# Kernel tuning notes

Measured on AMD Instinct MI355X. Metric: run time of the kernel, lower is better.

Reference implementation:

```python
import jax, jax.numpy as jnp
import numpy as np

C = 256
SCALE = 2
K = 3
GROUPS = 4


def _conv(x, w, b=None, groups=1, pad=0):
    y = jax.lax.conv_general_dilated(
        x, w, window_strides=(1, 1), padding=[(pad, pad), (pad, pad)],
        dimension_numbers=("NCHW", "OIHW", "NCHW"), feature_group_count=groups)
    if b is not None:
        y = y + b[None, :, None, None]
    return y


def _bn(x, g, b, m, v):
    # eval-mode BatchNorm2d, eps=1e-5
    scale = g / jnp.sqrt(v + 1e-5)
    return (x - m[None, :, None, None]) * scale[None, :, None, None] + b[None, :, None, None]


def _silu(x):
    return x * jax.nn.sigmoid(x)


def setup_inputs() -> dict:
    key = jax.random.key(0)
    ks = jax.random.split(key, 16)
    c = C
    s2k2 = SCALE ** 2 * K ** 2
    p = lambda k, shape, sc=0.05: jax.random.normal(k, shape, dtype=jnp.float32) * sc
    return {
        "x": jax.random.normal(ks[0], (8, c, 64, 64), dtype=jnp.float32),
        # kernel_compressor: 1x1, c -> c//2
        "Wkc": p(ks[1], (c // 2, c, 1, 1)), "bkc": p(ks[2], (c // 2,)),
        # kernel_predictor: 3x3 c//2 -> c//4, BN, SiLU, 1x1 -> s^2*k^2
        "Wkp1": p(ks[3], (c // 4, c // 2, 3, 3)), "bkp1": p(ks[4], (c // 4,)),
        "g1": 1.0 + p(ks[5], (c // 4,)), "be1": p(ks[6], (c // 4,)),
        "m1": p(ks[7], (c // 4,)), "v1": 1.0 + jax.random.uniform(ks[8], (c // 4,), dtype=jnp.float32),
        "Wkp2": p(ks[9], (s2k2, c // 4, 1, 1)), "bkp2": p(ks[10], (s2k2,)),
        # grouped 3x3 "deform" conv: c -> c, groups=4, no bias
        "Wdef": p(ks[11], (c, c // GROUPS, 3, 3)),
        # semantic gate
        "Wg1": p(ks[12], (c // 4, c, 1, 1)), "bg1": p(ks[13], (c // 4,)),
        "Wg2": p(ks[14], (c, c // 4, 1, 1)), "bg2": p(ks[15], (c,)),
    }


def reference(x, Wkc, bkc, Wkp1, bkp1, g1, be1, m1, v1, Wkp2, bkp2, Wdef, Wg1, bg1, Wg2, bg2):
    b, c, h, w = x.shape
    s, k = SCALE, K
    # --- dynamic reassembly kernel prediction ---
    comp = _conv(x, Wkc, bkc)                                    # (b, c/2, h, w)
    t = _silu(_bn(_conv(comp, Wkp1, bkp1, pad=1), g1, be1, m1, v1))
    kw = _conv(t, Wkp2, bkp2)                                    # (b, s^2*k^2, h, w)
    kw = kw.transpose(0, 2, 3, 1).reshape(b, h, w, s * s, k * k)
    kw = jax.nn.softmax(kw, axis=-1)
    # --- unfold (k x k patches, pad k//2), F.unfold ordering: kernel pos i*k+j ---
    xp = jnp.pad(x, ((0, 0), (0, 0), (1, 1), (1, 1)))
    patches = jnp.stack([xp[:, :, i:i + h, j:j + w]
                         for i in range(k) for j in range(k)], axis=-1)  # (b,c,h,w,k^2)
    kernel_out = jnp.einsum('bchwk,bhwsk->bhwsc', patches, kw)           # (b,h,w,s^2,c)
    kernel_out = kernel_out.transpose(0, 4, 1, 3, 2).reshape(b, c, h * s, w * s)
    # --- grouped conv branch + bilinear upsample (align_corners=False) ---
    enh = _conv(x, Wdef, None, groups=GROUPS, pad=1)
    up = jax.image.resize(enh, (b, c, h * s, w * s), method='linear')
    fused = kernel_out + up
    # --- SE-style semantic gate ---
    pooled = jnp.mean(fused, axis=(2, 3), keepdims=True)
    gate = jax.nn.sigmoid(_conv(_silu(_conv(pooled, Wg1, bg1)), Wg2, bg2))
    return fused * gate
```

## Files before the change

### kernel.cpp

```cpp
#include <hip/hip_runtime.h>
#include <hip/hip_bf16.h>

typedef __hip_bfloat16 bf16;
typedef __attribute__((ext_vector_type(8))) short short8;
typedef __attribute__((ext_vector_type(4))) float floatx4;

__device__ __forceinline__ float cvt(float v){ return v; }
__device__ __forceinline__ float cvt(bf16 v){ return __bfloat162float(v); }
__device__ __forceinline__ unsigned short f2bu(float f){
    union { float f; unsigned u; } uf; uf.f = f;
    unsigned u = uf.u;
    return (unsigned short)((u + 0x7FFFu + ((u>>16)&1u)) >> 16);
}
__device__ __forceinline__ float bu2f(unsigned short b){
    union { unsigned u; float f; } uf; uf.u = ((unsigned)b)<<16; return uf.f;
}
__device__ __forceinline__ floatx4 mfma16(short8 a, short8 b, floatx4 c){
    return __builtin_amdgcn_mfma_f32_16x16x32_bf16(a, b, c, 0, 0, 0);
}
__device__ __forceinline__ int swz8(int row, int part){
    return row*32 + ((part ^ ((row>>1)&3))<<3);
}
template<typename T>
__device__ __forceinline__ void ld4(const T* p, float& o0, float& o1, float& o2, float& o3){
    T t[4]; __builtin_memcpy(t, p, 4*sizeof(T));
    o0=cvt(t[0]); o1=cvt(t[1]); o2=cvt(t[2]); o3=cvt(t[3]);
}
__device__ __forceinline__ void ld2f(const float* p, float& o0, float& o1){
    float t[2]; __builtin_memcpy(t, p, 8);
    o0=t[0]; o1=t[1];
}

constexpr size_t O_KW    = 0;
constexpr size_t O_ENH   = O_KW    + 1179648;
constexpr size_t O_XBT   = O_ENH   + 8388608;
constexpr size_t O_COMPB = O_XBT   + 4194304;
constexpr size_t O_TB    = O_COMPB + 2097152;
constexpr size_t O_POOL  = O_TB    + 1048576;
constexpr size_t O_GATE  = O_POOL  + 2048;
constexpr size_t O_WKC   = O_GATE  + 2048;
constexpr size_t O_BKC   = O_WKC   + 32768;
constexpr size_t O_WKP1  = O_BKC   + 128;
constexpr size_t O_ALPHA = O_WKP1  + 73728;
constexpr size_t O_BETA  = O_ALPHA + 64;
constexpr size_t O_WKP2  = O_BETA  + 64;
constexpr size_t O_BKP2  = O_WKP2  + 2304;
constexpr size_t O_WDEF  = O_BKP2  + 64;
constexpr size_t O_WG1   = O_WDEF  + 147456;
constexpr size_t O_BG1   = O_WG1   + 16384;
constexpr size_t O_WG2   = O_BG1   + 64;
constexpr size_t O_BG2   = O_WG2   + 16384;
constexpr size_t O_FLAG  = O_BG2   + 256;
constexpr size_t O_WKCB  = (O_FLAG + 1 + 3) & ~(size_t)3;
constexpr size_t O_WKP1B = O_WKCB  + 16384;
constexpr size_t O_WDEFB = O_WKP1B + 36864;

__global__ __launch_bounds__(256) void kdet(const unsigned* __restrict__ w, float* flag)
{
    int hits = 0;
    for (int i = threadIdx.x; i < 16384; i += 256){
        unsigned v = w[i];
        hits += (((v >> 7) & 0xFFu) == 0xFFu) ? 1 : 0;
    }
    __shared__ int sh[256];
    sh[threadIdx.x] = hits;
    __syncthreads();
    for (int o = 128; o > 0; o >>= 1){
        if (threadIdx.x < o) sh[threadIdx.x] += sh[threadIdx.x + o];
        __syncthreads();
    }
    if (threadIdx.x == 0) flag[0] = (sh[0] > 0) ? 1.0f : 0.0f;
}

template<typename T>
__device__ __forceinline__ void k0_body(
    const T* Wkc, const T* bkc, const T* Wkp1, const T* bkp1,
    const T* g1, const T* be1, const T* m1, const T* v1,
    const T* Wkp2, const T* bkp2, const T* Wdef,
    const T* Wg1, const T* bg1, const T* Wg2, const T* bg2,
    float* ws)
{
    int i = blockIdx.x*256 + threadIdx.x;
    if (i < 32768){ ws[O_WKC+i] = cvt(Wkc[i]); return; }  i -= 32768;
    if (i < 128)  { ws[O_BKC+i] = cvt(bkc[i]); return; }  i -= 128;
    if (i < 73728){ ws[O_WKP1+i]= cvt(Wkp1[i]); return; } i -= 73728;
    if (i < 64){
        float a = cvt(g1[i]) / sqrtf(cvt(v1[i]) + 1e-5f);
        ws[O_ALPHA+i] = a;
        ws[O_BETA+i]  = (cvt(bkp1[i]) - cvt(m1[i]))*a + cvt(be1[i]);
        return;
    } i -= 64;
    if (i < 2304) { ws[O_WKP2+i] = cvt(Wkp2[i]); return; } i -= 2304;
    if (i < 36)   { ws[O_BKP2+i] = cvt(bkp2[i]); return; } i -= 36;
    if (i < 147456){ ws[O_WDEF+i]= cvt(Wdef[i]); return; } i -= 147456;
    if (i < 16384){ ws[O_WG1+i]  = cvt(Wg1[i]); return; }  i -= 16384;
    if (i < 64)   { ws[O_BG1+i]  = cvt(bg1[i]); return; }  i -= 64;
    if (i < 16384){ ws[O_WG2+i]  = cvt(Wg2[i]); return; }  i -= 16384;
    if (i < 256)  { ws[O_BG2+i]  = cvt(bg2[i]); return; }  i -= 256;
    if (i < 2048) { ws[O_POOL+i] = 0.f; return; }
}

__global__ __launch_bounds__(256) void k0_prep(
    const void* Wkc, const void* bkc, const void* Wkp1, const void* bkp1,
    const void* g1, const void* be1, const void* m1, const void* v1,
    const void* Wkp2, const void* bkp2, const void* Wdef,
    const void* Wg1, const void* bg1, const void* Wg2, const void* bg2,
    float* ws)
{
    if (ws[O_FLAG] > 0.5f)
        k0_body<float>((const float*)Wkc,(const float*)bkc,(const float*)Wkp1,(const float*)bkp1,
                       (const float*)g1,(const float*)be1,(const float*)m1,(const float*)v1,
                       (const float*)Wkp2,(const float*)bkp2,(const float*)Wdef,
                       (const float*)Wg1,(const float*)bg1,(const float*)Wg2,(const float*)bg2, ws);
    else
        k0_body<bf16>((const bf16*)Wkc,(const bf16*)bkc,(const bf16*)Wkp1,(const bf16*)bkp1,
                      (const bf16*)g1,(const bf16*)be1,(const bf16*)m1,(const bf16*)v1,
                      (const bf16*)Wkp2,(const bf16*)bkp2,(const bf16*)Wdef,
                      (const bf16*)Wg1,(const bf16*)bg1,(const bf16*)Wg2,(const bf16*)bg2, ws);
}

__global__ __launch_bounds__(256) void k0b_pack(float* ws)
{
    unsigned short* wkcb  = (unsigned short*)(ws + O_WKCB);
    unsigned short* wkp1b = (unsigned short*)(ws + O_WKP1B);
    unsigned short* wdefb = (unsigned short*)(ws + O_WDEFB);
    int i = blockIdx.x*256 + threadIdx.x;
    if (i < 32768){
        int kc = i>>12, cout = (i>>5)&127, cil = i&31;
        wkcb[i] = f2bu(ws[O_WKC + (size_t)cout*256 + kc*32 + cil]);
        return;
    } i -= 32768;
    if (i < 73728){
        int ch = i/18432, r = i - ch*18432;
        int kp = r>>11, cout = (r>>5)&63, cil = r&31;
        wkp1b[i] = f2bu(ws[O_WKP1 + ((size_t)cout*128 + ch*32 + cil)*9 + kp]);
        return;
    } i -= 73728;
    if (i < 147456){
        int g = i/36864, r1 = i - g*36864;
        int ch = r1/18432, r2 = r1 - ch*18432;
        int kp = r2>>11, cout = (r2>>5)&63, cil = r2&31;
        wdefb[i] = f2bu(ws[O_WDEF + (((size_t)(g*64+cout))*64 + ch*32 + cil)*9 + kp]);
    }
}

template<typename T>
__device__ __forceinline__ void xcvt_body(const T* __restrict__ x, unsigned short* __restrict__ xbt,
                                          float* lT)
{
    const int b = blockIdx.y;
    const int ci0 = (blockIdx.x & 3) * 64;
    const int pos0 = (blockIdx.x >> 2) * 64;
    const int lane = threadIdx.x & 63;
    const int wrow = threadIdx.x >> 6;
    for (int i = wrow; i < 64; i += 4)
        lT[i*65 + lane] = cvt(x[((size_t)(b*256 + ci0 + i))*4096 + pos0 + lane]);
    __syncthreads();
    for (int u = threadIdx.x; u < 2048; u += 256){
        const int pr = u >> 5, pc = u & 31;
        unsigned lo = f2bu(lT[(2*pc)*65 + pr]);
        unsigned hi = f2bu(lT[(2*pc+1)*65 + pr]);
        *(unsigned*)&xbt[((size_t)(b*4096) + pos0 + pr)*256 + ci0 + 2*pc] = lo | (hi<<16);
    }
}

__global__ __launch_bounds__(256) void xcvt(const void* x, unsigned short* xbt, const float* flag)
{
    __shared__ float lT[64*65];
    if (*flag > 0.5f) xcvt_body<float>((const float*)x, xbt, lT);
    else              xcvt_body<bf16>((const bf16*)x, xbt, lT);
}

__global__ __launch_bounds__(256) void k1_mfma(
    const unsigned short* __restrict__ xbt, const unsigned short* __restrict__ wb,
    const float* __restrict__ bias, unsigned short* __restrict__ compb)
{
    __shared__ __align__(16) short lA[128*32];
    __shared__ __align__(16) short lB[64*32];
    const int b = blockIdx.y, pos0 = blockIdx.x*64;
    const int tid = threadIdx.x;
    const int wave = tid>>6, lane = tid&63, q = lane>>4, r16 = lane&15;
    const int mh = (wave&1)*64, nh = (wave>>1)*32;
    floatx4 zero = {0.f,0.f,0.f,0.f};
    floatx4 acc[4][2];
    #pragma unroll
    for (int m=0;m<4;m++){ acc[m][0]=zero; acc[m][1]=zero; }

    for (int kc=0;kc<8;kc++){
        __syncthreads();
        {
            const short8* s = (const short8*)(wb + kc*4096);
            const int u0 = tid, u1 = tid + 256;
            *(short8*)&lA[swz8(u0>>2, u0&3)] = s[u0];
            *(short8*)&lA[swz8(u1>>2, u1&3)] = s[u1];
        }
        {
            const int p = tid>>2, part = tid&3;
            *(short8*)&lB[swz8(p, part)] =
                *(const short8*)(xbt + ((size_t)(b*4096)+pos0+p)*256 + kc*32 + part*8);
        }
        __syncthreads();
        short8 af[4], bfr[2];
        #pragma unroll
        for (int mt=0;mt<4;mt++) af[mt]  = *(const short8*)&lA[swz8(mh + mt*16 + r16, q)];
        #pragma unroll
        for (int nt=0;nt<2;nt++) bfr[nt] = *(const short8*)&lB[swz8(nh + nt*16 + r16, q)];
        #pragma unroll
        for (int mt=0;mt<4;mt++)
            #pragma unroll
            for (int nt=0;nt<2;nt++)
                acc[mt][nt] = mfma16(af[mt], bfr[nt], acc[mt][nt]);
    }
    #pragma unroll
    for (int mt=0;mt<4;mt++){
        const int cb = mh + mt*16 + q*4;
        const float b0=bias[cb], b1=bias[cb+1], b2=bias[cb+2], b3=bias[cb+3];
        #pragma unroll
        for (int nt=0;nt<2;nt++){
            const int pos = pos0 + nh + nt*16 + r16;
            floatx4 v = acc[mt][nt];
            uint2 pk;
            pk.x = (unsigned)f2bu(v.x+b0) | ((unsigned)f2bu(v.y+b1)<<16);
            pk.y = (unsigned)f2bu(v.z+b2) | ((unsigned)f2bu(v.w+b3)<<16);
            *(uint2*)(compb + ((size_t)(b*4096)+pos)*128 + cb) = pk;
        }
    }
}

__global__ __launch_bounds__(256) void conv3x3_all(
    const unsigned short* __restrict__ xbt, const unsigned short* __restrict__ compb,
    const unsigned short* __restrict__ wkp1b, const unsigned short* __restrict__ wdefb,
    const float* __restrict__ alpha, const float* __restrict__ beta,
    const float* __restrict__ Wkp2, const float* __restrict__ bkp2,
    float* __restrict__ kw, float* __restrict__ enh)
{
    __shared__ __align__(16) short lXT[18432];
    __shared__ float wl[2340];
    const int row0 = blockIdx.x*4, b = blockIdx.y, z = blockIdx.z;
    const bool isKP = (z == 0);
    const int g = isKP ? 0 : (z-1);
    const int CICH  = isKP ? 4 : 2;
    const int CITOT = isKP ? 128 : 256;
    const int cibase = g*64;
    const unsigned short* src  = isKP ? compb : xbt;
    const unsigned short* wsrc = isKP ? wkp1b : (wdefb + (size_t)g*36864);
    const int tid = threadIdx.x;
    const int wave = tid>>6, lane = tid&63, q = lane>>4, r16 = lane&15;
    floatx4 zero = {0.f,0.f,0.f,0.f};
    floatx4 acc[4][4];
    #pragma unroll
    for (int m=0;m<4;m++){ acc[m][0]=zero; acc[m][1]=zero; acc[m][2]=zero; acc[m][3]=zero; }

    {
        short8 zz = {0,0,0,0,0,0,0,0};
        short8* d = (short8*)lXT;
        for (int i = tid; i < 1584; i += 256) d[i] = zz;
    }
    if (isKP){
        for (int i = tid; i < 2340; i += 256)
            wl[i] = (i < 2304) ? Wkp2[i] : bkp2[i-2304];
    }

    for (int ch = 0; ch < CICH; ch++){
        __syncthreads();
        {
            const int gc = tid>>2, part = tid&3;
            #pragma unroll
            for (int r=0;r<6;r++){
                const int gr = row0 - 1 + r;
                if ((unsigned)gr < 64u){
                    const unsigned short* sp = src +
                        ((size_t)(b*4096) + gr*64 + gc)*CITOT + cibase + ch*32 + part*8;
                    *(short8*)&lXT[swz8(r*66 + 1 + gc, part)] = *(const short8*)sp;
                }
            }
        }
        __syncthreads();
        const unsigned short* wch = wsrc + ch*18432;
        #pragma unroll
        for (int kp=0; kp<9; kp++){
            const int dr = kp/3, dc = kp - dr*3;
            short8 af[4], bfr[4];
            #pragma unroll
            for (int mt=0;mt<4;mt++)
                af[mt] = *(const short8*)(wch + (kp*64 + mt*16 + r16)*32 + q*8);
            #pragma unroll
            for (int nt=0;nt<4;nt++)
                bfr[nt] = *(const short8*)&lXT[swz8((wave+dr)*66 + nt*16 + r16 + dc, q)];
            #pragma unroll
            for (int mt=0;mt<4;mt++)
                #pragma unroll
                for (int nt=0;nt<4;nt++)
                    acc[mt][nt] = mfma16(af[mt], bfr[nt], acc[mt][nt]);
        }
    }
    if (isKP){
        __syncthreads();
        #pragma unroll
        for (int mt=0;mt<4;mt++){
            const int cb = mt*16 + q*4;
            const float a0=alpha[cb],a1=alpha[cb+1],a2=alpha[cb+2],a3=alpha[cb+3];
            const float e0=beta[cb],e1=beta[cb+1],e2=beta[cb+2],e3=beta[cb+3];
            #pragma unroll
            for (int nt=0;nt<4;nt++){
                const int pl = wave*64 + nt*16 + r16;
                floatx4 v = acc[mt][nt];
                float z0=v.x*a0+e0, z1=v.y*a1+e1, z2=v.z*a2+e2, z3=v.w*a3+e3;
                z0 = z0/(1.f+expf(-z0)); z1 = z1/(1.f+expf(-z1));
                z2 = z2/(1.f+expf(-z2)); z3 = z3/(1.f+expf(-z3));
                uint2 pk;
                pk.x = (unsigned)f2bu(z0) | ((unsigned)f2bu(z1)<<16);
                pk.y = (unsigned)f2bu(z2) | ((unsigned)f2bu(z3)<<16);
                *(uint2*)&lXT[pl*72 + cb] = pk;
            }
        }
        __syncthreads();
        const unsigned short* tp = (const unsigned short*)&lXT[tid*72];
        float acc36[36];
        #pragma unroll
        for (int o=0;o<36;o++) acc36[o] = wl[2304+o];
        #pragma unroll
        for (int c8=0;c8<8;c8++){
            short8 v8 = *(const short8*)(tp + c8*8);
            float f[8];
            #pragma unroll
            for (int j=0;j<8;j++) f[j] = bu2f((unsigned short)v8[j]);
            #pragma unroll
            for (int jj=0;jj<8;jj++){
                const int ci = c8*8+jj;
                #pragma unroll
                for (int o=0;o<36;o++) acc36[o] += f[jj]*wl[o*64+ci];
            }
        }
        const int gid = b*4096 + (row0 + (tid>>6))*64 + (tid&63);
        float* op = kw + (size_t)gid*36;
        #pragma unroll
        for (int s=0;s<4;s++){
            float mx = acc36[s*9];
            #pragma unroll
            for (int k=1;k<9;k++) mx = fmaxf(mx, acc36[s*9+k]);
            float e[9]; float sum=0.f;
            #pragma unroll
            for (int k=0;k<9;k++){ e[k]=expf(acc36[s*9+k]-mx); sum+=e[k]; }
            float inv = 1.f/sum;
            #pragma unroll
            for (int k=0;k<9;k++) op[s*9+k] = e[k]*inv;
        }
    } else {
        const int orow = row0 + wave;
        #pragma unroll
        for (int mt=0;mt<4;mt++){
            #pragma unroll
            for (int nt=0;nt<4;nt++){
                const int pos = orow*64 + nt*16 + r16;
                floatx4 v = acc[mt][nt];
                float* op = enh + ((size_t)(b*256) + g*64 + mt*16 + q*4)*4096 + pos;
                op[0]=v.x; op[4096]=v.y; op[8192]=v.z; op[12288]=v.w;
            }
        }
    }
}

template<typename T>
__device__ __forceinline__ void k5_body(
    const T* __restrict__ x, const float* __restrict__ kw,
    const float* __restrict__ enh, float* __restrict__ out,
    float* __restrict__ pooled, float* kwl)
{
    const int hi = blockIdx.x & 63;
    const int b  = blockIdx.x >> 6;
    const int c0 = blockIdx.y * 64;
    for (int i=threadIdx.x;i<2304;i+=256){
        int wi = i/36, r = i - wi*36;
        kwl[wi*37+r] = kw[((size_t)(b*4096 + hi*64 + wi))*36 + r];
    }
    __syncthreads();
    const int lane = threadIdx.x & 63;
    const int wv   = threadIdx.x >> 6;
    const int a    = lane & 31;
    const int hsel = lane >> 5;

    float k0r[36], k1r[36];
    #pragma unroll
    for (int r=0;r<36;r++) k0r[r] = kwl[(2*a)*37+r];
    #pragma unroll
    for (int r=0;r<36;r++) k1r[r] = kwl[(2*a+1)*37+r];

    const bool vy0 = hi>0, vy2 = hi<63;
    const int rm = vy0? hi-1 : 0;
    const int rp = vy2? hi+1 : 63;
    const int y0 = hi*2;
    const bool e0 = (a==0), e31 = (a==31);
    const int xb = e0 ? 0 : (e31 ? 60 : (2*a-1));
    const int eAb = e0 ? 0 : a-1;
    const int eBb = 31 + a;
    const int eAr = a+1;
    const int eBr = e31 ? 63 : 33+a;

    for (int it=0; it<8; ++it){
        const int c = c0 + (wv<<1) + hsel + (it<<3);
        const T* xc = x + ((size_t)(b*256)+c)*4096 + hi*64 + xb;
        float g[3][4];
        ld4(xc, g[1][0], g[1][1], g[1][2], g[1][3]);
        if (vy0) ld4(xc-64, g[0][0], g[0][1], g[0][2], g[0][3]);
        else     { g[0][0]=0.f; g[0][1]=0.f; g[0][2]=0.f; g[0][3]=0.f; }
        if (vy2) ld4(xc+64, g[2][0], g[2][1], g[2][2], g[2][3]);
        else     { g[2][0]=0.f; g[2][1]=0.f; g[2][2]=0.f; g[2][3]=0.f; }
        float w0[3][4];
        #pragma unroll
        for (int i=0;i<3;i++){
            float g0=g[i][0], g1=g[i][1], g2=g[i][2], g3=g[i][3];
            w0[i][0] = e0 ? 0.f : (e31 ? g1 : g0);
            w0[i][1] = e0 ? g0  : (e31 ? g2 : g1);
            w0[i][2] = e0 ? g1  : (e31 ? g3 : g2);
            w0[i][3] = e0 ? g2  : (e31 ? 0.f : g3);
        }
        float ko[2][4];
        #pragma unroll
        for (int s=0;s<4;s++){
            float a0c = 0.f, a1c = 0.f;
            #pragma unroll
            for (int i=0;i<3;i++){
                a0c += w0[i][0]*k0r[s*9+3*i] + w0[i][1]*k0r[s*9+3*i+1] + w0[i][2]*k0r[s*9+3*i+2];
                a1c += w0[i][1]*k1r[s*9+3*i] + w0[i][2]*k1r[s*9+3*i+1] + w0[i][3]*k1r[s*9+3*i+2];
            }
            ko[0][s]=a0c; ko[1][s]=a1c;
        }
        const float* ec = enh + ((size_t)(b*256)+c)*4096;
        float hAe[3], hAo[3], hBe[3], hBo[3];
        const int rows[3] = {rm, hi, rp};
        #pragma unroll
        for (int i=0;i<3;i++){
            const float* er = ec + rows[i]*64;
            float fA0, fA1; ld2f(er + eAb, fA0, fA1);
            float vAl = fA0, vAc = e0 ? fA0 : fA1;
            float vAr = er[eAr];
            float fB0, fB1; ld2f(er + eBb, fB0, fB1);
            float vBr = er[eBr];
            hAe[i] = 0.25f*vAl + 0.75f*vAc;
            hAo[i] = 0.75f*vAc + 0.25f*vAr;
            hBe[i] = 0.25f*fB0 + 0.75f*fB1;
            hBo[i] = 0.75f*fB1 + 0.25f*vBr;
        }
        float uAe0 = 0.25f*hAe[0] + 0.75f*hAe[1], uAe1 = 0.75f*hAe[1] + 0.25f*hAe[2];
        float uAo0 = 0.25f*hAo[0] + 0.75f*hAo[1], uAo1 = 0.75f*hAo[1] + 0.25f*hAo[2];
        float uBe0 = 0.25f*hBe[0] + 0.75f*hBe[1], uBe1 = 0.75f*hBe[1] + 0.25f*hBe[2];
        float uBo0 = 0.25f*hBo[0] + 0.75f*hBo[1], uBo1 = 0.75f*hBo[1] + 0.25f*hBo[2];
        float o00 = ko[0][0]+uAe0, o01 = ko[1][0]+uAo0;
        float o02 = ko[0][1]+uBe0, o03 = ko[1][1]+uBo0;
        float o10 = ko[0][2]+uAe1, o11 = ko[1][2]+uAo1;
        float o12 = ko[0][3]+uBe1, o13 = ko[1][3]+uBo1;
        float* o = out + (((size_t)(b*256)+c)*128 + y0)*128;
        *(float2*)(o + 2*a)        = make_float2(o00, o01);
        *(float2*)(o + 64 + 2*a)   = make_float2(o02, o03);
        *(float2*)(o + 128 + 2*a)  = make_float2(o10, o11);
        *(float2*)(o + 192 + 2*a)  = make_float2(o12, o13);
        float ps = (o00+o01) + (o02+o03) + (o10+o11) + (o12+o13);
        ps += __shfl_down(ps,16,32); ps += __shfl_down(ps, 8,32);
        ps += __shfl_down(ps, 4,32); ps += __shfl_down(ps, 2,32);
        ps += __shfl_down(ps, 1,32);
        if (a==0) atomicAdd(&pooled[b*256 + c], ps);
    }
}

__global__ __launch_bounds__(256) void k5_fuse(
    const void* x, const float* kw, const float* enh, float* out,
    float* pooled, const float* flag)
{
    __shared__ float kwl[64*37];
    if (*flag > 0.5f) k5_body<float>((const float*)x, kw, enh, out, pooled, kwl);
    else              k5_body<bf16>((const bf16*)x, kw, enh, out, pooled, kwl);
}

__global__ __launch_bounds__(256) void k7_gate(
    const float* __restrict__ pooled,
    const float* __restrict__ Wg1, const float* __restrict__ bg1,
    const float* __restrict__ Wg2, const float* __restrict__ bg2,
    float* __restrict__ gate)
{
    const int b = blockIdx.x;
    __shared__ float pl[256];
    __shared__ float hid[64];
    pl[threadIdx.x] = pooled[b*256+threadIdx.x] * (1.f/16384.f);
    __syncthreads();
    if (threadIdx.x < 64){
        float a = bg1[threadIdx.x];
        const float* w = Wg1 + (size_t)threadIdx.x*256;
        for (int c=0;c<256;c++) a += w[c]*pl[c];
        hid[threadIdx.x] = a/(1.f+expf(-a));
    }
    __syncthreads();
    float a = bg2[threadIdx.x];
    const float* w = Wg2 + (size_t)threadIdx.x*64;
    for (int j=0;j<64;j++) a += w[j]*hid[j];
    gate[b*256+threadIdx.x] = 1.f/(1.f+expf(-a));
}

__global__ __launch_bounds__(256) void k8_scale(
    float* __restrict__ out, const float* __restrict__ gate)
{
    float4* p = (float4*)out;
    for (size_t gid = (size_t)blockIdx.x*256 + threadIdx.x; gid < 8388608u; gid += 524288u){
        const float g = gate[gid>>12];
        float4 v = p[gid];
        v.x*=g; v.y*=g; v.z*=g; v.w*=g;
        p[gid] = v;
    }
}

extern "C" void kernel_launch(void* const* d_in, const int* in_sizes, int n_in,
                              void* d_out, int out_size, void* d_ws, size_t ws_size,
                              hipStream_t stream)
{
    float* ws = (float*)d_ws;
    float* out = (float*)d_out;
    unsigned short* xbt   = (unsigned short*)(ws + O_XBT);
    unsigned short* compb = (unsigned short*)(ws + O_COMPB);
    unsigned short* wkcb  = (unsigned short*)(ws + O_WKCB);
    unsigned short* wkp1b = (unsigned short*)(ws + O_WKP1B);
    unsigned short* wdefb = (unsigned short*)(ws + O_WDEFB);

    kdet<<<1, 256, 0, stream>>>((const unsigned*)d_in[1], ws + O_FLAG);
    k0_prep<<<1140, 256, 0, stream>>>(d_in[1],d_in[2],d_in[3],d_in[4],d_in[5],d_in[6],d_in[7],d_in[8],
                                      d_in[9],d_in[10],d_in[11],d_in[12],d_in[13],d_in[14],d_in[15], ws);
    k0b_pack<<<992, 256, 0, stream>>>(ws);
    xcvt<<<dim3(256,8), 256, 0, stream>>>(d_in[0], xbt, ws+O_FLAG);
    k1_mfma<<<dim3(64,8), 256, 0, stream>>>(xbt, wkcb, ws+O_BKC, compb);
    conv3x3_all<<<dim3(16,8,5), 256, 0, stream>>>(xbt, compb, wkp1b, wdefb,
                                                  ws+O_ALPHA, ws+O_BETA,
                                                  ws+O_WKP2, ws+O_BKP2,
                                                  ws+O_KW, ws+O_ENH);
    k5_fuse<<<dim3(512,4), 256, 0, stream>>>(d_in[0], ws+O_KW, ws+O_ENH, out, ws+O_POOL, ws+O_FLAG);
    k7_gate<<<8, 256, 0, stream>>>(ws+O_POOL, ws+O_WG1, ws+O_BG1, ws+O_WG2, ws+O_BG2, ws+O_GATE);
    k8_scale<<<2048, 256, 0, stream>>>(out, ws+O_GATE);
}
```

Baseline: 397.3 us.

## Stage 3x3 conv weights in LDS and widen 1x1 conv position tile

In the 3x3 conv kernel, each input-channel chunk of weights is now copied once into a swizzled shared-memory buffer. The four waves read their MFMA A-fragments from that buffer instead of each issuing its own global load. The 1x1 compressor kernel now handles 128 positions per block instead of 64, with a 4x4 accumulator tile per wave, which halves the grid and reuses each staged weight tile twice as much. The trade-off is much higher LDS use in the conv kernel, which may reduce occupancy. The reused SiLU staging buffer also gets a 76-element row stride that is not 16-byte aligned for vector reads.

```diff
diff --git a/kernel.cpp b/kernel.cpp
--- a/kernel.cpp
+++ b/kernel.cpp
@@ -176,15 +176,15 @@
     const float* __restrict__ bias, unsigned short* __restrict__ compb)
 {
     __shared__ __align__(16) short lA[128*32];
-    __shared__ __align__(16) short lB[64*32];
-    const int b = blockIdx.y, pos0 = blockIdx.x*64;
+    __shared__ __align__(16) short lB[128*32];
+    const int b = blockIdx.y, pos0 = blockIdx.x*128;
     const int tid = threadIdx.x;
     const int wave = tid>>6, lane = tid&63, q = lane>>4, r16 = lane&15;
-    const int mh = (wave&1)*64, nh = (wave>>1)*32;
+    const int mh = (wave&1)*64, nh = (wave>>1)*64;
     floatx4 zero = {0.f,0.f,0.f,0.f};
-    floatx4 acc[4][2];
+    floatx4 acc[4][4];
     #pragma unroll
-    for (int m=0;m<4;m++){ acc[m][0]=zero; acc[m][1]=zero; }
+    for (int m=0;m<4;m++){ acc[m][0]=zero; acc[m][1]=zero; acc[m][2]=zero; acc[m][3]=zero; }
 
     for (int kc=0;kc<8;kc++){
         __syncthreads();
@@ -195,20 +195,24 @@
             *(short8*)&lA[swz8(u1>>2, u1&3)] = s[u1];
         }
         {
-            const int p = tid>>2, part = tid&3;
-            *(short8*)&lB[swz8(p, part)] =
-                *(const short8*)(xbt + ((size_t)(b*4096)+pos0+p)*256 + kc*32 + part*8);
-        }
-        __syncthreads();
-        short8 af[4], bfr[2];
+            #pragma unroll
+            for (int k=0;k<2;k++){
+                const int u = tid + k*256;
+                const int p = u>>2, part = u&3;
+                *(short8*)&lB[swz8(p, part)] =
+                    *(const short8*)(xbt + ((size_t)(b*4096)+pos0+p)*256 + kc*32 + part*8);
+            }
+        }
+        __syncthreads();
+        short8 af[4], bfr[4];
         #pragma unroll
         for (int mt=0;mt<4;mt++) af[mt]  = *(const short8*)&lA[swz8(mh + mt*16 + r16, q)];
         #pragma unroll
-        for (int nt=0;nt<2;nt++) bfr[nt] = *(const short8*)&lB[swz8(nh + nt*16 + r16, q)];
+        for (int nt=0;nt<4;nt++) bfr[nt] = *(const short8*)&lB[swz8(nh + nt*16 + r16, q)];
         #pragma unroll
         for (int mt=0;mt<4;mt++)
             #pragma unroll
-            for (int nt=0;nt<2;nt++)
+            for (int nt=0;nt<4;nt++)
                 acc[mt][nt] = mfma16(af[mt], bfr[nt], acc[mt][nt]);
     }
     #pragma unroll
@@ -216,7 +220,7 @@
         const int cb = mh + mt*16 + q*4;
         const float b0=bias[cb], b1=bias[cb+1], b2=bias[cb+2], b3=bias[cb+3];
         #pragma unroll
-        for (int nt=0;nt<2;nt++){
+        for (int nt=0;nt<4;nt++){
             const int pos = pos0 + nh + nt*16 + r16;
             floatx4 v = acc[mt][nt];
             uint2 pk;
@@ -234,7 +238,8 @@
     const float* __restrict__ Wkp2, const float* __restrict__ bkp2,
     float* __restrict__ kw, float* __restrict__ enh)
 {
-    __shared__ __align__(16) short lXT[18432];
+    __shared__ __align__(16) short lX[6*66*32];
+    __shared__ __align__(16) short lW[19456];
     __shared__ float wl[2340];
     const int row0 = blockIdx.x*4, b = blockIdx.y, z = blockIdx.z;
     const bool isKP = (z == 0);
@@ -253,7 +258,7 @@
 
     {
         short8 zz = {0,0,0,0,0,0,0,0};
-        short8* d = (short8*)lXT;
+        short8* d = (short8*)lX;
         for (int i = tid; i < 1584; i += 256) d[i] = zz;
     }
     if (isKP){
@@ -263,6 +268,14 @@
 
     for (int ch = 0; ch < CICH; ch++){
         __syncthreads();
+        {
+            const short8* s = (const short8*)(wsrc + ch*18432);
+            #pragma unroll
+            for (int i=0;i<9;i++){
+                const int u = tid + i*256;
+                *(short8*)&lW[swz8(u>>2, u&3)] = s[u];
+            }
+        }
         {
             const int gc = tid>>2, part = tid&3;
             #pragma unroll
@@ -271,22 +284,21 @@
                 if ((unsigned)gr < 64u){
                     const unsigned short* sp = src +
                         ((size_t)(b*4096) + gr*64 + gc)*CITOT + cibase + ch*32 + part*8;
-                    *(short8*)&lXT[swz8(r*66 + 1 + gc, part)] = *(const short8*)sp;
+                    *(short8*)&lX[swz8(r*66 + 1 + gc, part)] = *(const short8*)sp;
                 }
             }
         }
         __syncthreads();
-        const unsigned short* wch = wsrc + ch*18432;
         #pragma unroll
         for (int kp=0; kp<9; kp++){
             const int dr = kp/3, dc = kp - dr*3;
             short8 af[4], bfr[4];
             #pragma unroll
             for (int mt=0;mt<4;mt++)
-                af[mt] = *(const short8*)(wch + (kp*64 + mt*16 + r16)*32 + q*8);
+                af[mt] = *(const short8*)&lW[swz8(kp*64 + mt*16 + r16, q)];
             #pragma unroll
             for (int nt=0;nt<4;nt++)
-                bfr[nt] = *(const short8*)&lXT[swz8((wave+dr)*66 + nt*16 + r16 + dc, q)];
+                bfr[nt] = *(const short8*)&lX[swz8((wave+dr)*66 + nt*16 + r16 + dc, q)];
             #pragma unroll
             for (int mt=0;mt<4;mt++)
                 #pragma unroll
@@ -311,11 +323,11 @@
                 uint2 pk;
                 pk.x = (unsigned)f2bu(z0) | ((unsigned)f2bu(z1)<<16);
                 pk.y = (unsigned)f2bu(z2) | ((unsigned)f2bu(z3)<<16);
-                *(uint2*)&lXT[pl*72 + cb] = pk;
-            }
-        }
-        __syncthreads();
-        const unsigned short* tp = (const unsigned short*)&lXT[tid*72];
+                *(uint2*)&lW[pl*76 + cb] = pk;
+            }
+        }
+        __syncthreads();
+        const unsigned short* tp = (const unsigned short*)&lW[tid*76];
         float acc36[36];
         #pragma unroll
         for (int o=0;o<36;o++) acc36[o] = wl[2304+o];
@@ -525,7 +537,7 @@
                                       d_in[9],d_in[10],d_in[11],d_in[12],d_in[13],d_in[14],d_in[15], ws);
     k0b_pack<<<992, 256, 0, stream>>>(ws);
     xcvt<<<dim3(256,8), 256, 0, stream>>>(d_in[0], xbt, ws+O_FLAG);
-    k1_mfma<<<dim3(64,8), 256, 0, stream>>>(xbt, wkcb, ws+O_BKC, compb);
+    k1_mfma<<<dim3(32,8), 256, 0, stream>>>(xbt, wkcb, ws+O_BKC, compb);
     conv3x3_all<<<dim3(16,8,5), 256, 0, stream>>>(xbt, compb, wkp1b, wdefb,
                                                   ws+O_ALPHA, ws+O_BETA,
                                                   ws+O_WKP2, ws+O_BKP2,
```

Measured after the change: 355.7 us. 10.5% less time.
